# Performance work log

Measured on AMD Instinct MI355X. Metric: run time of the kernel, lower is better.

Reference implementation:

```python
import jax, jax.numpy as jnp
import numpy as np

B, T, D = 16, 2048, 256

def setup_inputs() -> dict:
    key = jax.random.key(0)
    k1, k2, k3 = jax.random.split(key, 3)
    q = jax.random.normal(k1, (B, T, D), dtype=jnp.float32)
    a = jax.random.normal(k2, (B, T, D), dtype=jnp.float32)
    # original uses 'uniform' init; scale ~ small
    U = jax.random.uniform(k3, (D, D), dtype=jnp.float32, minval=-0.05, maxval=0.05)
    return {"q": q, "a": a, "U": U}

def reference(q, a, U):
    # G[b,i,j] = tanh( (q[b,i,:] @ U) . a[b,j,:] )
    qU = jnp.einsum('btd,de->bte', q, U)                 # [B,Tq,D]
    G = jnp.tanh(jnp.einsum('btd,bsd->bts', qU, a))      # [B,Tq,Ta]
    g_q = jax.nn.softmax(jnp.max(G, axis=-1), axis=1)    # [B,Tq]
    g_a = jax.nn.softmax(jnp.max(G, axis=1), axis=1)     # [B,Ta]
    q_out = jnp.einsum('btd,bt->bd', q, g_q)             # [B,D]
    a_out = jnp.einsum('bsd,bs->bd', a, g_a)             # [B,D]
    return (q_out, a_out)
```

## Files before the change

### kernel.cpp

```cpp
#include <hip/hip_runtime.h>
#include <stdint.h>

typedef __attribute__((ext_vector_type(8))) short s8v;
typedef __attribute__((ext_vector_type(4))) float f4v;

__device__ __forceinline__ unsigned short f2bf(float f) {
  unsigned u = __float_as_uint(f);
  u = u + 0x7FFFu + ((u >> 16) & 1u);
  return (unsigned short)(u >> 16);
}
__device__ __forceinline__ unsigned encf(float f) {
  unsigned i = __float_as_uint(f);
  return (i & 0x80000000u) ? ~i : (i | 0x80000000u);
}
__device__ __forceinline__ float decf(unsigned u) {
  unsigned i = (u & 0x80000000u) ? (u & 0x7FFFFFFFu) : ~u;
  return __uint_as_float(i);
}
__device__ __forceinline__ void gload_lds16(const unsigned short* g, unsigned short* l) {
  __builtin_amdgcn_global_load_lds((const __attribute__((address_space(1))) void*)g,
                                   (__attribute__((address_space(3))) void*)l, 16, 0, 0);
}

__global__ void convert_qa_kernel(const float4* __restrict__ q, const float4* __restrict__ a,
                                  ushort4* __restrict__ qb, ushort4* __restrict__ ab) {
  const int i = blockIdx.x * 256 + threadIdx.x;
  float4 v = q[i];
  qb[i] = make_ushort4(f2bf(v.x), f2bf(v.y), f2bf(v.z), f2bf(v.w));
  float4 w = a[i];
  ab[i] = make_ushort4(f2bf(w.x), f2bf(w.y), f2bf(w.z), f2bf(w.w));
}

__global__ void convert_u_kernel(const float* __restrict__ U, unsigned short* __restrict__ Ut) {
  const int k = blockIdx.x;
  const int n = threadIdx.x;
  Ut[n * 256 + k] = f2bf(U[k * 256 + n]);
}

template<int MODE>
__global__ void gemm_bt(const unsigned short* __restrict__ A,
                        const unsigned short* __restrict__ Bm,
                        long strideA, long strideB,
                        unsigned short* __restrict__ C,
                        unsigned* __restrict__ rowmax,
                        unsigned* __restrict__ colmax) {
  __shared__ unsigned short As[128 * 64];
  __shared__ unsigned short Bs[128 * 64];
  __shared__ unsigned rowLds[128];
  __shared__ unsigned colLds[128];

  const int tid  = threadIdx.x;
  const int tm   = blockIdx.x, tn = blockIdx.y, b = blockIdx.z;
  const unsigned short* Ab = A + (long)b * strideA + (long)tm * 128 * 256;
  const unsigned short* Bb = Bm + (long)b * strideB + (long)tn * 128 * 256;

  const int lane = tid & 63;
  const int m16  = lane & 15;
  const int quad = lane >> 4;
  const int wave = tid >> 6;
  const int wm   = wave >> 1, wn = wave & 1;
  const int srow = tid >> 3;
  const int scol = (tid & 7) * 8;

  if (MODE == 1 && tid < 128) { rowLds[tid] = 0u; colLds[tid] = 0u; }

  f4v acc[4][4] = {};

  for (int kt = 0; kt < 4; ++kt) {
    const int k0 = kt * 64;
    __syncthreads();
    #pragma unroll
    for (int i = 0; i < 4; ++i) {
      const int r = i * 32 + srow;
      gload_lds16(Ab + (long)r * 256 + k0 + scol, &As[i * 2048 + tid * 8]);
    }
    #pragma unroll
    for (int i = 0; i < 4; ++i) {
      const int r = i * 32 + srow;
      gload_lds16(Bb + (long)r * 256 + k0 + scol, &Bs[i * 2048 + tid * 8]);
    }
    __syncthreads();
    #pragma unroll
    for (int kk = 0; kk < 2; ++kk) {
      const int ko = kk * 32 + quad * 8;
      s8v af[4], bfv[4];
      #pragma unroll
      for (int i = 0; i < 4; ++i) af[i] = *(const s8v*)&As[(wm * 64 + i * 16 + m16) * 64 + ko];
      #pragma unroll
      for (int j = 0; j < 4; ++j) bfv[j] = *(const s8v*)&Bs[(wn * 64 + j * 16 + m16) * 64 + ko];
      #pragma unroll
      for (int i = 0; i < 4; ++i)
        #pragma unroll
        for (int j = 0; j < 4; ++j)
          acc[i][j] = __builtin_amdgcn_mfma_f32_16x16x32_bf16(af[i], bfv[j], acc[i][j], 0, 0, 0);
    }
  }

  if (MODE == 0) {
    #pragma unroll
    for (int i = 0; i < 4; ++i)
      #pragma unroll
      for (int r = 0; r < 4; ++r) {
        const long row = (long)tm * 128 + wm * 64 + i * 16 + quad * 4 + r;
        #pragma unroll
        for (int j = 0; j < 4; ++j) {
          const int col = tn * 128 + wn * 64 + j * 16 + m16;
          C[row * 256 + col] = f2bf(acc[i][j][r]);
        }
      }
  } else {
    #pragma unroll
    for (int i = 0; i < 4; ++i)
      #pragma unroll
      for (int r = 0; r < 4; ++r) {
        float v = fmaxf(fmaxf(acc[i][0][r], acc[i][1][r]), fmaxf(acc[i][2][r], acc[i][3][r]));
        #pragma unroll
        for (int d2 = 1; d2 < 16; d2 <<= 1) v = fmaxf(v, __shfl_xor(v, d2));
        if (m16 == 0) atomicMax(&rowLds[wm * 64 + i * 16 + quad * 4 + r], encf(v));
      }
    #pragma unroll
    for (int j = 0; j < 4; ++j) {
      float v = -3.4e38f;
      #pragma unroll
      for (int i = 0; i < 4; ++i)
        #pragma unroll
        for (int r = 0; r < 4; ++r) v = fmaxf(v, acc[i][j][r]);
      v = fmaxf(v, __shfl_xor(v, 16));
      v = fmaxf(v, __shfl_xor(v, 32));
      if (quad == 0) atomicMax(&colLds[wn * 64 + j * 16 + m16], encf(v));
    }
    __syncthreads();
    if (tid < 128) {
      atomicMax(&rowmax[(long)b * 2048 + tm * 128 + tid], rowLds[tid]);
    } else {
      atomicMax(&colmax[(long)b * 2048 + tn * 128 + (tid - 128)], colLds[tid - 128]);
    }
  }
}

__global__ void softmax_kernel(const unsigned* __restrict__ rowmax, const unsigned* __restrict__ colmax,
                               float* __restrict__ gq, float* __restrict__ ga) {
  const int b = blockIdx.x;
  const unsigned* e = blockIdx.y ? colmax : rowmax;
  float* g = blockIdx.y ? ga : gq;
  const int tid = threadIdx.x;
  float x[8];
  float m = -3.4e38f;
  #pragma unroll
  for (int j = 0; j < 8; ++j) {
    x[j] = tanhf(decf(e[b * 2048 + j * 256 + tid]));
    m = fmaxf(m, x[j]);
  }
  #pragma unroll
  for (int d2 = 1; d2 < 64; d2 <<= 1) m = fmaxf(m, __shfl_xor(m, d2));
  __shared__ float sred[4];
  __shared__ float sred2[4];
  if ((tid & 63) == 0) sred[tid >> 6] = m;
  __syncthreads();
  m = fmaxf(fmaxf(sred[0], sred[1]), fmaxf(sred[2], sred[3]));
  float s = 0.f;
  #pragma unroll
  for (int j = 0; j < 8; ++j) { x[j] = expf(x[j] - m); s += x[j]; }
  #pragma unroll
  for (int d2 = 1; d2 < 64; d2 <<= 1) s += __shfl_xor(s, d2);
  if ((tid & 63) == 0) sred2[tid >> 6] = s;
  __syncthreads();
  s = sred2[0] + sred2[1] + sred2[2] + sred2[3];
  const float inv = 1.f / s;
  #pragma unroll
  for (int j = 0; j < 8; ++j) g[b * 2048 + j * 256 + tid] = x[j] * inv;
}

__global__ void wsum_kernel(const float* __restrict__ q, const float* __restrict__ a,
                            const float* __restrict__ gq, const float* __restrict__ ga,
                            float* __restrict__ out) {
  const int d = threadIdx.x;
  const int chunk = blockIdx.x;
  const int b = blockIdx.y;
  const int z = blockIdx.z;
  const float* src = z ? a : q;
  const float* g = z ? ga : gq;
  float acc = 0.f;
  const int t0 = chunk * 128;
  const float* srow = src + ((long)b * 2048 + t0) * 256 + d;
  const float* grow = g + b * 2048 + t0;
  #pragma unroll 8
  for (int t = 0; t < 128; ++t) acc += srow[(long)t * 256] * grow[t];
  atomicAdd(&out[z * 4096 + b * 256 + d], acc);
}

extern "C" void kernel_launch(void* const* d_in, const int* in_sizes, int n_in,
                              void* d_out, int out_size, void* d_ws, size_t ws_size,
                              hipStream_t stream) {
  const float* q = (const float*)d_in[0];
  const float* a = (const float*)d_in[1];
  const float* U = (const float*)d_in[2];
  float* out = (float*)d_out;

  char* w = (char*)d_ws;
  unsigned short* qb = (unsigned short*)w;
  unsigned short* ab = (unsigned short*)(w + (16ull << 20));
  unsigned short* qU = (unsigned short*)(w + (32ull << 20));
  unsigned short* Ut = (unsigned short*)(w + (48ull << 20));
  unsigned* rmax = (unsigned*)(w + (48ull << 20) + (128ull << 10));
  unsigned* cmax = rmax + 32768;
  float* gq = (float*)(cmax + 32768);
  float* ga = gq + 32768;

  hipMemsetAsync(rmax, 0, 2 * 32768 * sizeof(unsigned), stream);
  hipMemsetAsync(out, 0, 8192 * sizeof(float), stream);

  convert_qa_kernel<<<8192, 256, 0, stream>>>((const float4*)q, (const float4*)a,
                                              (ushort4*)qb, (ushort4*)ab);
  convert_u_kernel<<<256, 256, 0, stream>>>(U, Ut);

  gemm_bt<0><<<dim3(256, 2, 1), 256, 0, stream>>>(qb, Ut, 0, 0, qU, nullptr, nullptr);

  gemm_bt<1><<<dim3(16, 16, 16), 256, 0, stream>>>(qU, ab, 2048 * 256, 2048 * 256,
                                                   nullptr, rmax, cmax);

  softmax_kernel<<<dim3(16, 2), 256, 0, stream>>>(rmax, cmax, gq, ga);
  wsum_kernel<<<dim3(16, 16, 2), 256, 0, stream>>>(q, a, gq, ga, out);
}
```

Before: 189.9 us.

## Swizzle LDS tiles, fuse softmax into weighted sum, read bf16 copies

Applies an XOR swizzle to the shared-memory tile layout in the GEMM so that MFMA operand reads avoid LDS bank conflicts. The separate softmax kernel is folded into the weighted-sum kernel: each block recomputes the full-row max and sum and its own chunk of weights, which removes one launch and the gq/ga round trip. The weighted sum now reads the bf16 copies of q and a with vectorized loads instead of the fp32 originals, halving the bytes read. In exchange the softmax reduction is repeated in every block, and bf16 inputs reduce the precision of the outputs.

```diff
diff --git a/kernel.cpp b/kernel.cpp
--- a/kernel.cpp
+++ b/kernel.cpp
@@ -8,6 +8,9 @@
   unsigned u = __float_as_uint(f);
   u = u + 0x7FFFu + ((u >> 16) & 1u);
   return (unsigned short)(u >> 16);
+}
+__device__ __forceinline__ float bf2f(unsigned short h) {
+  return __uint_as_float((unsigned)h << 16);
 }
 __device__ __forceinline__ unsigned encf(float f) {
   unsigned i = __float_as_uint(f);
@@ -37,32 +40,40 @@
   Ut[n * 256 + k] = f2bf(U[k * 256 + n]);
 }
 
-template<int MODE>
+template<int WM, int WN, int MODE>
 __global__ void gemm_bt(const unsigned short* __restrict__ A,
                         const unsigned short* __restrict__ Bm,
                         long strideA, long strideB,
                         unsigned short* __restrict__ C,
                         unsigned* __restrict__ rowmax,
                         unsigned* __restrict__ colmax) {
-  __shared__ unsigned short As[128 * 64];
-  __shared__ unsigned short Bs[128 * 64];
-  __shared__ unsigned rowLds[128];
-  __shared__ unsigned colLds[128];
+  constexpr int T = WM * WN * 64;
+  constexpr int AROWS = WM * 64;
+  constexpr int BROWS = WN * 64;
+  constexpr int RPI = T / 8;
+
+  __shared__ unsigned short As[AROWS * 64];
+  __shared__ unsigned short Bs[BROWS * 64];
+  __shared__ unsigned rowLds[AROWS];
+  __shared__ unsigned colLds[BROWS];
 
   const int tid  = threadIdx.x;
   const int tm   = blockIdx.x, tn = blockIdx.y, b = blockIdx.z;
-  const unsigned short* Ab = A + (long)b * strideA + (long)tm * 128 * 256;
-  const unsigned short* Bb = Bm + (long)b * strideB + (long)tn * 128 * 256;
+  const unsigned short* Ab = A + (long)b * strideA + (long)tm * AROWS * 256;
+  const unsigned short* Bb = Bm + (long)b * strideB + (long)tn * BROWS * 256;
 
   const int lane = tid & 63;
   const int m16  = lane & 15;
   const int quad = lane >> 4;
   const int wave = tid >> 6;
-  const int wm   = wave >> 1, wn = wave & 1;
+  const int wm   = wave / WN, wn = wave % WN;
   const int srow = tid >> 3;
-  const int scol = (tid & 7) * 8;
-
-  if (MODE == 1 && tid < 128) { rowLds[tid] = 0u; colLds[tid] = 0u; }
+  const int scol = (((tid & 7) ^ (srow & 7))) * 8;
+
+  if (MODE == 1) {
+    if (tid < AROWS) rowLds[tid] = 0u;
+    if (tid < BROWS) colLds[tid] = 0u;
+  }
 
   f4v acc[4][4] = {};
 
@@ -70,24 +81,26 @@
     const int k0 = kt * 64;
     __syncthreads();
     #pragma unroll
-    for (int i = 0; i < 4; ++i) {
-      const int r = i * 32 + srow;
-      gload_lds16(Ab + (long)r * 256 + k0 + scol, &As[i * 2048 + tid * 8]);
-    }
-    #pragma unroll
-    for (int i = 0; i < 4; ++i) {
-      const int r = i * 32 + srow;
-      gload_lds16(Bb + (long)r * 256 + k0 + scol, &Bs[i * 2048 + tid * 8]);
+    for (int i = 0; i < AROWS / RPI; ++i) {
+      const int r = i * RPI + srow;
+      gload_lds16(Ab + (long)r * 256 + k0 + scol, &As[i * RPI * 64 + tid * 8]);
+    }
+    #pragma unroll
+    for (int i = 0; i < BROWS / RPI; ++i) {
+      const int r = i * RPI + srow;
+      gload_lds16(Bb + (long)r * 256 + k0 + scol, &Bs[i * RPI * 64 + tid * 8]);
     }
     __syncthreads();
     #pragma unroll
     for (int kk = 0; kk < 2; ++kk) {
-      const int ko = kk * 32 + quad * 8;
+      const int cs = ((kk * 4 + quad) ^ (m16 & 7)) * 8;
       s8v af[4], bfv[4];
       #pragma unroll
-      for (int i = 0; i < 4; ++i) af[i] = *(const s8v*)&As[(wm * 64 + i * 16 + m16) * 64 + ko];
-      #pragma unroll
-      for (int j = 0; j < 4; ++j) bfv[j] = *(const s8v*)&Bs[(wn * 64 + j * 16 + m16) * 64 + ko];
+      for (int i = 0; i < 4; ++i)
+        af[i] = *(const s8v*)&As[(wm * 64 + i * 16 + m16) * 64 + cs];
+      #pragma unroll
+      for (int j = 0; j < 4; ++j)
+        bfv[j] = *(const s8v*)&Bs[(wn * 64 + j * 16 + m16) * 64 + cs];
       #pragma unroll
       for (int i = 0; i < 4; ++i)
         #pragma unroll
@@ -101,10 +114,10 @@
     for (int i = 0; i < 4; ++i)
       #pragma unroll
       for (int r = 0; r < 4; ++r) {
-        const long row = (long)tm * 128 + wm * 64 + i * 16 + quad * 4 + r;
+        const long row = (long)tm * AROWS + wm * 64 + i * 16 + quad * 4 + r;
         #pragma unroll
         for (int j = 0; j < 4; ++j) {
-          const int col = tn * 128 + wn * 64 + j * 16 + m16;
+          const int col = tn * BROWS + wn * 64 + j * 16 + m16;
           C[row * 256 + col] = f2bf(acc[i][j][r]);
         }
       }
@@ -130,20 +143,29 @@
       if (quad == 0) atomicMax(&colLds[wn * 64 + j * 16 + m16], encf(v));
     }
     __syncthreads();
-    if (tid < 128) {
-      atomicMax(&rowmax[(long)b * 2048 + tm * 128 + tid], rowLds[tid]);
-    } else {
-      atomicMax(&colmax[(long)b * 2048 + tn * 128 + (tid - 128)], colLds[tid - 128]);
-    }
-  }
-}
-
-__global__ void softmax_kernel(const unsigned* __restrict__ rowmax, const unsigned* __restrict__ colmax,
-                               float* __restrict__ gq, float* __restrict__ ga) {
-  const int b = blockIdx.x;
-  const unsigned* e = blockIdx.y ? colmax : rowmax;
-  float* g = blockIdx.y ? ga : gq;
+    if (tid < AROWS) {
+      atomicMax(&rowmax[(long)b * 2048 + tm * AROWS + tid], rowLds[tid]);
+    } else if (tid < AROWS + BROWS) {
+      atomicMax(&colmax[(long)b * 2048 + tn * BROWS + (tid - AROWS)], colLds[tid - AROWS]);
+    }
+  }
+}
+
+__global__ void wsum_kernel(const ushort4* __restrict__ qb, const ushort4* __restrict__ ab,
+                            const unsigned* __restrict__ rowmax, const unsigned* __restrict__ colmax,
+                            float* __restrict__ out) {
   const int tid = threadIdx.x;
+  const int chunk = blockIdx.x;
+  const int b = blockIdx.y;
+  const int z = blockIdx.z;
+  const unsigned* e = z ? colmax : rowmax;
+  const ushort4* src = z ? ab : qb;
+
+  __shared__ float sm[4];
+  __shared__ float ss[4];
+  __shared__ float wLds[128];
+  __shared__ float red[256 * 4];
+
   float x[8];
   float m = -3.4e38f;
   #pragma unroll
@@ -153,40 +175,45 @@
   }
   #pragma unroll
   for (int d2 = 1; d2 < 64; d2 <<= 1) m = fmaxf(m, __shfl_xor(m, d2));
-  __shared__ float sred[4];
-  __shared__ float sred2[4];
-  if ((tid & 63) == 0) sred[tid >> 6] = m;
-  __syncthreads();
-  m = fmaxf(fmaxf(sred[0], sred[1]), fmaxf(sred[2], sred[3]));
+  if ((tid & 63) == 0) sm[tid >> 6] = m;
+  __syncthreads();
+  m = fmaxf(fmaxf(sm[0], sm[1]), fmaxf(sm[2], sm[3]));
   float s = 0.f;
   #pragma unroll
-  for (int j = 0; j < 8; ++j) { x[j] = expf(x[j] - m); s += x[j]; }
+  for (int j = 0; j < 8; ++j) s += expf(x[j] - m);
   #pragma unroll
   for (int d2 = 1; d2 < 64; d2 <<= 1) s += __shfl_xor(s, d2);
-  if ((tid & 63) == 0) sred2[tid >> 6] = s;
-  __syncthreads();
-  s = sred2[0] + sred2[1] + sred2[2] + sred2[3];
-  const float inv = 1.f / s;
-  #pragma unroll
-  for (int j = 0; j < 8; ++j) g[b * 2048 + j * 256 + tid] = x[j] * inv;
-}
-
-__global__ void wsum_kernel(const float* __restrict__ q, const float* __restrict__ a,
-                            const float* __restrict__ gq, const float* __restrict__ ga,
-                            float* __restrict__ out) {
-  const int d = threadIdx.x;
-  const int chunk = blockIdx.x;
-  const int b = blockIdx.y;
-  const int z = blockIdx.z;
-  const float* src = z ? a : q;
-  const float* g = z ? ga : gq;
-  float acc = 0.f;
-  const int t0 = chunk * 128;
-  const float* srow = src + ((long)b * 2048 + t0) * 256 + d;
-  const float* grow = g + b * 2048 + t0;
-  #pragma unroll 8
-  for (int t = 0; t < 128; ++t) acc += srow[(long)t * 256] * grow[t];
-  atomicAdd(&out[z * 4096 + b * 256 + d], acc);
+  if ((tid & 63) == 0) ss[tid >> 6] = s;
+  __syncthreads();
+  const float inv = 1.f / (ss[0] + ss[1] + ss[2] + ss[3]);
+
+  if (tid < 128) {
+    float xv = tanhf(decf(e[b * 2048 + chunk * 128 + tid]));
+    wLds[tid] = expf(xv - m) * inv;
+  }
+  __syncthreads();
+
+  const int dg = tid & 63;
+  const int rg = tid >> 6;
+  float a0 = 0.f, a1 = 0.f, a2 = 0.f, a3 = 0.f;
+  const long rowbase = (long)b * 2048 + chunk * 128;
+  for (int t = rg; t < 128; t += 4) {
+    const float w = wLds[t];
+    ushort4 v = src[(rowbase + t) * 64 + dg];
+    a0 += w * bf2f(v.x); a1 += w * bf2f(v.y);
+    a2 += w * bf2f(v.z); a3 += w * bf2f(v.w);
+  }
+  red[tid * 4 + 0] = a0; red[tid * 4 + 1] = a1;
+  red[tid * 4 + 2] = a2; red[tid * 4 + 3] = a3;
+  __syncthreads();
+  if (tid < 64) {
+    #pragma unroll
+    for (int k = 0; k < 4; ++k) {
+      float v = red[(0 * 64 + tid) * 4 + k] + red[(1 * 64 + tid) * 4 + k] +
+                red[(2 * 64 + tid) * 4 + k] + red[(3 * 64 + tid) * 4 + k];
+      atomicAdd(&out[z * 4096 + b * 256 + tid * 4 + k], v);
+    }
+  }
 }
 
 extern "C" void kernel_launch(void* const* d_in, const int* in_sizes, int n_in,
@@ -204,8 +231,6 @@
   unsigned short* Ut = (unsigned short*)(w + (48ull << 20));
   unsigned* rmax = (unsigned*)(w + (48ull << 20) + (128ull << 10));
   unsigned* cmax = rmax + 32768;
-  float* gq = (float*)(cmax + 32768);
-  float* ga = gq + 32768;
 
   hipMemsetAsync(rmax, 0, 2 * 32768 * sizeof(unsigned), stream);
   hipMemsetAsync(out, 0, 8192 * sizeof(float), stream);
@@ -214,11 +239,11 @@
                                               (ushort4*)qb, (ushort4*)ab);
   convert_u_kernel<<<256, 256, 0, stream>>>(U, Ut);
 
-  gemm_bt<0><<<dim3(256, 2, 1), 256, 0, stream>>>(qb, Ut, 0, 0, qU, nullptr, nullptr);
-
-  gemm_bt<1><<<dim3(16, 16, 16), 256, 0, stream>>>(qU, ab, 2048 * 256, 2048 * 256,
-                                                   nullptr, rmax, cmax);
-
-  softmax_kernel<<<dim3(16, 2), 256, 0, stream>>>(rmax, cmax, gq, ga);
-  wsum_kernel<<<dim3(16, 16, 2), 256, 0, stream>>>(q, a, gq, ga, out);
-}
+  gemm_bt<2, 2, 0><<<dim3(256, 2, 1), 256, 0, stream>>>(qb, Ut, 0, 0, qU, nullptr, nullptr);
+
+  gemm_bt<2, 2, 1><<<dim3(16, 16, 16), 256, 0, stream>>>(qU, ab, 2048 * 256, 2048 * 256,
+                                                         nullptr, rmax, cmax);
+
+  wsum_kernel<<<dim3(16, 16, 2), 256, 0, stream>>>((const ushort4*)qb, (const ushort4*)ab,
+                                                   rmax, cmax, out);
+}
```

Result: faster. 183.7 us (-3.3%).
